# Kernel tuning notes

Measured on AMD Instinct MI355X. Metric: run time of the kernel, lower is better.

Reference implementation:

```python
import jax, jax.numpy as jnp
import numpy as np

B, S, H, D = 32, 512, 768, 64  # batch, seq_len, hidden_size, inner_dim
BIG = 1e12


def _rope(x, sin_pos, cos_pos):
    # x: [B,S,D]; rotate pairs: [-x1, x0, -x3, x2, ...]
    x2 = jnp.stack([-x[..., 1::2], x[..., ::2]], axis=-1).reshape(x.shape)
    return x * cos_pos + x2 * sin_pos


def setup_inputs() -> dict:
    key = jax.random.key(0)
    k1, k2, k3 = jax.random.split(key, 3)
    hidden = jax.random.normal(k1, (B, S, H), dtype=jnp.float32)
    attention_mask = jnp.ones((B, S), dtype=jnp.float32)
    span_ids = jax.random.randint(k2, (B, S, S), 0, 2).astype(jnp.int32)
    dense_w = jax.random.normal(k3, (H, 2 * D), dtype=jnp.float32) * 0.02
    dense_b = jnp.zeros((2 * D,), dtype=jnp.float32)
    return {"hidden": hidden, "attention_mask": attention_mask,
            "span_ids": span_ids, "dense_w": dense_w, "dense_b": dense_b}


def reference(hidden, attention_mask, span_ids, dense_w, dense_b):
    b, s, _ = hidden.shape
    out = hidden @ dense_w + dense_b            # [B,S,2D]
    qw, kw = out[..., :D], out[..., D:]
    # sinusoidal position embedding, interleaved [s0,c0,s1,c1,...]
    pos = jnp.arange(s, dtype=jnp.float32)[:, None]              # [S,1]
    inv_freq = 10000.0 ** (-2.0 * jnp.arange(D // 2, dtype=jnp.float32) / D)
    ang = pos * inv_freq                                         # [S,D/2]
    sin_pos = jnp.repeat(jnp.sin(ang), 2, axis=-1)[None]         # [1,S,D]
    cos_pos = jnp.repeat(jnp.cos(ang), 2, axis=-1)[None]
    qw = _rope(qw, sin_pos, cos_pos)
    kw = _rope(kw, sin_pos, cos_pos)
    logits = jnp.einsum('bmd,bnd->bmn', qw, kw)                  # [B,S,S]
    pad = attention_mask[:, None, :]                             # mask keys (n)
    logits = logits * pad - (1.0 - pad) * BIG
    tril = jnp.tril(jnp.ones((s, s), logits.dtype), -1)          # strict lower
    logits = logits - tril * BIG
    logits = logits / (D ** 0.5)
    # multilabel categorical crossentropy over rows [B*S, S]
    y_true = span_ids.astype(logits.dtype).reshape(b * s, -1)
    y_pred = logits.reshape(b * s, -1)
    yp = (1.0 - 2.0 * y_true) * y_pred
    zeros = jnp.zeros((b * s, 1), yp.dtype)
    y_neg = jnp.concatenate([yp - y_true * BIG, zeros], axis=-1)
    y_pos = jnp.concatenate([yp - (1.0 - y_true) * BIG, zeros], axis=-1)
    loss = (jax.nn.logsumexp(y_neg, axis=-1) + jax.nn.logsumexp(y_pos, axis=-1)).mean()
    return loss
```

## Files before the change

kernel.cpp:

```cpp
#include <hip/hip_runtime.h>
#include <hip/hip_bf16.h>
#include <math.h>

#define Bb   32
#define Ss   512
#define Hh   768
#define Dd   64
#define ND   128
#define Mrows (Bb*Ss)
#define BIGF 1.0e12f

typedef __attribute__((ext_vector_type(8))) short short8;
typedef __attribute__((ext_vector_type(4))) float floatx4;

__device__ __forceinline__ short f2bf(float x) {
    unsigned u = __builtin_bit_cast(unsigned, x);
    u = (u + 0x7FFF + ((u >> 16) & 1)) >> 16;
    return (short)u;
}

__global__ __launch_bounds__(256) void prep_kernel(
    const float* __restrict__ w, short* __restrict__ wT,
    float2* __restrict__ rt)
{
    int idx = blockIdx.x * 256 + threadIdx.x;
    int k = idx >> 7;
    int n = idx & 127;
    wT[n * Hh + k] = f2bf(w[idx]);
    if (idx < Ss * 32) {
        int spos = idx >> 5;
        int i    = idx & 31;
        float ln_base = -logf(10000.0f) / 32.0f;
        float invf = expf(ln_base * (float)i);
        float sn, cs;
        sincosf((float)spos * invf, &sn, &cs);
        rt[idx] = make_float2(sn, cs);
    }
}

__global__ __launch_bounds__(256) void proj_rope_kernel(
    const float*  __restrict__ hidden,
    const short*  __restrict__ wT,
    const float*  __restrict__ bias,
    const float2* __restrict__ rt,
    short* __restrict__ qbf,
    short* __restrict__ kbf)
{
    const int tid   = threadIdx.x;
    const int w     = tid >> 6;
    const int lane  = tid & 63;
    const int quad  = lane >> 4;
    const int l15   = lane & 15;
    const int h     = w & 1;
    const int mrow0 = blockIdx.x * 32 + (w >> 1) * 16;

    const float* ap  = hidden + (size_t)(mrow0 + l15) * Hh + quad * 8;
    const short* bp0 = wT + (size_t)(h * 64 + l15) * Hh + quad * 8;

    floatx4 acc[4] = {{0.f,0.f,0.f,0.f},{0.f,0.f,0.f,0.f},
                      {0.f,0.f,0.f,0.f},{0.f,0.f,0.f,0.f}};

    float4 A0[2], A1[2];
    short8 Bf[2][4];

#define PLOAD(buf, kofs) do {                                   \
    A0[buf] = *(const float4*)(ap + (kofs));                    \
    A1[buf] = *(const float4*)(ap + (kofs) + 4);                \
    Bf[buf][0] = *(const short8*)(bp0 + (kofs));                \
    Bf[buf][1] = *(const short8*)(bp0 + 16 * Hh + (kofs));      \
    Bf[buf][2] = *(const short8*)(bp0 + 32 * Hh + (kofs));      \
    Bf[buf][3] = *(const short8*)(bp0 + 48 * Hh + (kofs));      \
} while (0)

#define PCOMP(buf) do {                                         \
    short8 av;                                                  \
    av[0] = f2bf(A0[buf].x); av[1] = f2bf(A0[buf].y);           \
    av[2] = f2bf(A0[buf].z); av[3] = f2bf(A0[buf].w);           \
    av[4] = f2bf(A1[buf].x); av[5] = f2bf(A1[buf].y);           \
    av[6] = f2bf(A1[buf].z); av[7] = f2bf(A1[buf].w);           \
    acc[0] = __builtin_amdgcn_mfma_f32_16x16x32_bf16(av, Bf[buf][0], acc[0], 0, 0, 0); \
    acc[1] = __builtin_amdgcn_mfma_f32_16x16x32_bf16(av, Bf[buf][1], acc[1], 0, 0, 0); \
    acc[2] = __builtin_amdgcn_mfma_f32_16x16x32_bf16(av, Bf[buf][2], acc[2], 0, 0, 0); \
    acc[3] = __builtin_amdgcn_mfma_f32_16x16x32_bf16(av, Bf[buf][3], acc[3], 0, 0, 0); \
} while (0)

    PLOAD(0, 0);
    #pragma unroll
    for (int cc = 0; cc < 12; ++cc) {
        if (2 * cc + 1 < 24) PLOAD(1, (2 * cc + 1) * 32);
        PCOMP(0);
        if (2 * cc + 2 < 24) PLOAD(0, (2 * cc + 2) * 32);
        PCOMP(1);
    }
#undef PLOAD
#undef PCOMP

    short* dst = h ? kbf : qbf;
    const float* bptr = bias + h * 64;

    #pragma unroll
    for (int t = 0; t < 4; ++t) {
        const int d  = t * 16 + l15;
        const float bz = bptr[d];
        const float2* rtp = rt + (d >> 1);
        #pragma unroll
        for (int reg = 0; reg < 4; ++reg) {
            const int grow = mrow0 + quad * 4 + reg;
            const int spos = grow & (Ss - 1);
            float2 sc = rtp[spos * 32];
            float x  = acc[t][reg] + bz;
            float xo = __shfl_xor(x, 1);
            float o  = (d & 1) ? (x * sc.y + xo * sc.x)
                               : (x * sc.y - xo * sc.x);
            dst[(size_t)grow * Dd + d] = f2bf(o);
        }
    }
}

__global__ __launch_bounds__(512) void span_loss_kernel(
    const short* __restrict__ qbf,
    const short* __restrict__ kbf,
    const float* __restrict__ mask,
    const int*   __restrict__ span,
    double* __restrict__ rowsum)
{
    const int b    = blockIdx.x >> 4;
    const int m0   = (blockIdx.x & 15) * 32;
    const int tid  = threadIdx.x;
    const int w    = tid >> 6;
    const int lane = tid & 63;
    const int quad = lane >> 4;
    const int l15  = lane & 15;
    const int rh   = w & 1;
    const int cg   = w >> 1;
    const int rbase = m0 + rh * 16;
    const int cbase = cg * 128;

    __shared__ float part[2][4][32];
    __shared__ float bred[2][32];

    const short* qp = qbf + (size_t)(b * Ss + rbase + l15) * Dd + quad * 8;
    short8 a0 = *(const short8*)(qp);
    short8 a1 = *(const short8*)(qp + 32);

    floatx4 acc[8];
    #pragma unroll
    for (int t = 0; t < 8; ++t) acc[t] = (floatx4){0.f, 0.f, 0.f, 0.f};

    const short* kp = kbf + (size_t)(b * Ss + cbase + l15) * Dd + quad * 8;
    #pragma unroll
    for (int t = 0; t < 8; ++t) {
        short8 bv = *(const short8*)(kp + (size_t)t * 16 * Dd);
        acc[t] = __builtin_amdgcn_mfma_f32_16x16x32_bf16(a0, bv, acc[t], 0, 0, 0);
    }
    #pragma unroll
    for (int t = 0; t < 8; ++t) {
        short8 bv = *(const short8*)(kp + (size_t)t * 16 * Dd + 32);
        acc[t] = __builtin_amdgcn_mfma_f32_16x16x32_bf16(a1, bv, acc[t], 0, 0, 0);
    }

    unsigned spb = 0;
    #pragma unroll
    for (int t = 0; t < 8; ++t) {
        const int n = cbase + t * 16 + l15;
        const float pd = mask[b * Ss + n];
        #pragma unroll
        for (int reg = 0; reg < 4; ++reg) {
            const int m = rbase + quad * 4 + reg;
            const int sv = span[((size_t)(b * Ss + m)) * Ss + n];
            float logit = acc[t][reg] * pd - (1.0f - pd) * BIGF;
            if (n < m) logit -= BIGF;
            logit *= 0.125f;
            float ft = (float)sv;
            acc[t][reg] = (1.0f - 2.0f * ft) * logit;
            spb |= (unsigned)(sv != 0) << (t * 4 + reg);
        }
    }

    float mxn[4] = {0.f, 0.f, 0.f, 0.f};
    float mxp[4] = {0.f, 0.f, 0.f, 0.f};
    #pragma unroll
    for (int t = 0; t < 8; ++t) {
        #pragma unroll
        for (int reg = 0; reg < 4; ++reg) {
            float ft = (float)((spb >> (t * 4 + reg)) & 1u);
            float yp = acc[t][reg];
            mxn[reg] = fmaxf(mxn[reg], yp - ft * BIGF);
            mxp[reg] = fmaxf(mxp[reg], yp - (1.0f - ft) * BIGF);
        }
    }
    #pragma unroll
    for (int off = 1; off < 16; off <<= 1) {
        #pragma unroll
        for (int reg = 0; reg < 4; ++reg) {
            mxn[reg] = fmaxf(mxn[reg], __shfl_xor(mxn[reg], off));
            mxp[reg] = fmaxf(mxp[reg], __shfl_xor(mxp[reg], off));
        }
    }
    if (l15 == 0) {
        #pragma unroll
        for (int reg = 0; reg < 4; ++reg) {
            part[0][cg][rh * 16 + quad * 4 + reg] = mxn[reg];
            part[1][cg][rh * 16 + quad * 4 + reg] = mxp[reg];
        }
    }
    __syncthreads();
    if (tid < 64) {
        int np = tid >> 5, r = tid & 31;
        float mv = fmaxf(fmaxf(part[np][0][r], part[np][1][r]),
                         fmaxf(part[np][2][r], part[np][3][r]));
        bred[np][r] = mv;
    }
    __syncthreads();

    float bmn[4], bmp[4];
    #pragma unroll
    for (int reg = 0; reg < 4; ++reg) {
        bmn[reg] = bred[0][rh * 16 + quad * 4 + reg];
        bmp[reg] = bred[1][rh * 16 + quad * 4 + reg];
    }
    float smn[4] = {0.f, 0.f, 0.f, 0.f};
    float smp[4] = {0.f, 0.f, 0.f, 0.f};
    #pragma unroll
    for (int t = 0; t < 8; ++t) {
        #pragma unroll
        for (int reg = 0; reg < 4; ++reg) {
            float ft = (float)((spb >> (t * 4 + reg)) & 1u);
            float yp = acc[t][reg];
            smn[reg] += __expf(yp - ft * BIGF - bmn[reg]);
            smp[reg] += __expf(yp - (1.0f - ft) * BIGF - bmp[reg]);
        }
    }
    #pragma unroll
    for (int off = 1; off < 16; off <<= 1) {
        #pragma unroll
        for (int reg = 0; reg < 4; ++reg) {
            smn[reg] += __shfl_xor(smn[reg], off);
            smp[reg] += __shfl_xor(smp[reg], off);
        }
    }
    if (l15 == 0) {
        #pragma unroll
        for (int reg = 0; reg < 4; ++reg) {
            part[0][cg][rh * 16 + quad * 4 + reg] = smn[reg];
            part[1][cg][rh * 16 + quad * 4 + reg] = smp[reg];
        }
    }
    __syncthreads();

    if (tid < 32) {
        int r = tid;
        float SN = __expf(-bred[0][r])
                 + part[0][0][r] + part[0][1][r] + part[0][2][r] + part[0][3][r];
        float SP = __expf(-bred[1][r])
                 + part[1][0][r] + part[1][1][r] + part[1][2][r] + part[1][3][r];
        float lse = (bred[0][r] + logf(SN)) + (bred[1][r] + logf(SP));
        rowsum[(size_t)(b * Ss + m0 + r)] = (double)lse;
    }
}

__global__ __launch_bounds__(1024) void final_reduce_kernel(
    const double* __restrict__ rowsum, float* __restrict__ out)
{
    __shared__ double sh[1024];
    const int tid = threadIdx.x;
    double s = 0.0;
    #pragma unroll
    for (int i = 0; i < 16; ++i) s += rowsum[tid + i * 1024];
    sh[tid] = s;
    __syncthreads();
    for (int off = 512; off > 0; off >>= 1) {
        if (tid < off) sh[tid] += sh[tid + off];
        __syncthreads();
    }
    if (tid == 0) out[0] = (float)(sh[0] / (double)Mrows);
}

extern "C" void kernel_launch(void* const* d_in, const int* in_sizes, int n_in,
                              void* d_out, int out_size, void* d_ws, size_t ws_size,
                              hipStream_t stream)
{
    const float* hidden = (const float*)d_in[0];
    const float* mask   = (const float*)d_in[1];
    const int*   span   = (const int*)  d_in[2];
    const float* w      = (const float*)d_in[3];
    const float* bias   = (const float*)d_in[4];
    float* out = (float*)d_out;

    char* p = (char*)d_ws;
    double* rowsum = (double*)p;            p += 131072;
    short*  wT     = (short*)p;             p += 196608;
    float2* rt     = (float2*)p;            p += 131072;
    short*  qbf    = (short*)p;             p += (size_t)Mrows * Dd * 2;
    short*  kbf    = (short*)p;

    prep_kernel<<<Hh * ND / 256, 256, 0, stream>>>(w, wT, rt);
    proj_rope_kernel<<<Mrows / 32, 256, 0, stream>>>(hidden, wT, bias, rt, qbf, kbf);
    span_loss_kernel<<<Bb * 16, 512, 0, stream>>>(qbf, kbf, mask, span, rowsum);
    final_reduce_kernel<<<1, 1024, 0, stream>>>(rowsum, out);
}
```

Measured before the change: 158.5 us.

## Pre-swizzle weights into MFMA fragment order and prefetch span loads early

The prep kernel now writes the bf16 weights in the exact per-lane MFMA fragment layout, so each wave in the projection reads its B operand as one contiguous 1KB chunk per step instead of strided rows. The span loss kernel issues all span_ids and mask loads before the QK MFMAs, so the dominant span read overlaps with compute. Launch-bound occupancy hints are added to both kernels. Hoisting the span loads raises register pressure (32 ints per thread), which could conflict with the 4-block occupancy target.

```diff
diff --git a/kernel.cpp b/kernel.cpp
--- a/kernel.cpp
+++ b/kernel.cpp
@@ -20,13 +20,18 @@
 }
 
 __global__ __launch_bounds__(256) void prep_kernel(
-    const float* __restrict__ w, short* __restrict__ wT,
+    const float* __restrict__ w, short* __restrict__ wfrag,
     float2* __restrict__ rt)
 {
     int idx = blockIdx.x * 256 + threadIdx.x;
-    int k = idx >> 7;
-    int n = idx & 127;
-    wT[n * Hh + k] = f2bf(w[idx]);
+    int j    = idx & 7;
+    int lane = (idx >> 3) & 63;
+    int rest = idx >> 9;
+    int c    = rest % 24;
+    int tt   = rest / 24;
+    int n    = tt * 16 + (lane & 15);
+    int k    = c * 32 + (lane >> 4) * 8 + j;
+    wfrag[idx] = f2bf(w[k * ND + n]);
     if (idx < Ss * 32) {
         int spos = idx >> 5;
         int i    = idx & 31;
@@ -38,9 +43,9 @@
     }
 }
 
-__global__ __launch_bounds__(256) void proj_rope_kernel(
+__global__ __launch_bounds__(256, 2) void proj_rope_kernel(
     const float*  __restrict__ hidden,
-    const short*  __restrict__ wT,
+    const short*  __restrict__ wfrag,
     const float*  __restrict__ bias,
     const float2* __restrict__ rt,
     short* __restrict__ qbf,
@@ -55,7 +60,7 @@
     const int mrow0 = blockIdx.x * 32 + (w >> 1) * 16;
 
     const float* ap  = hidden + (size_t)(mrow0 + l15) * Hh + quad * 8;
-    const short* bp0 = wT + (size_t)(h * 64 + l15) * Hh + quad * 8;
+    const short* bp0 = wfrag + (size_t)(h * 4) * 24 * 512 + lane * 8;
 
     floatx4 acc[4] = {{0.f,0.f,0.f,0.f},{0.f,0.f,0.f,0.f},
                       {0.f,0.f,0.f,0.f},{0.f,0.f,0.f,0.f}};
@@ -63,13 +68,13 @@
     float4 A0[2], A1[2];
     short8 Bf[2][4];
 
-#define PLOAD(buf, kofs) do {                                   \
-    A0[buf] = *(const float4*)(ap + (kofs));                    \
-    A1[buf] = *(const float4*)(ap + (kofs) + 4);                \
-    Bf[buf][0] = *(const short8*)(bp0 + (kofs));                \
-    Bf[buf][1] = *(const short8*)(bp0 + 16 * Hh + (kofs));      \
-    Bf[buf][2] = *(const short8*)(bp0 + 32 * Hh + (kofs));      \
-    Bf[buf][3] = *(const short8*)(bp0 + 48 * Hh + (kofs));      \
+#define PLOAD(buf, c) do {                                        \
+    A0[buf] = *(const float4*)(ap + (c) * 32);                    \
+    A1[buf] = *(const float4*)(ap + (c) * 32 + 4);                \
+    Bf[buf][0] = *(const short8*)(bp0 + 0 * 24 * 512 + (c) * 512);\
+    Bf[buf][1] = *(const short8*)(bp0 + 1 * 24 * 512 + (c) * 512);\
+    Bf[buf][2] = *(const short8*)(bp0 + 2 * 24 * 512 + (c) * 512);\
+    Bf[buf][3] = *(const short8*)(bp0 + 3 * 24 * 512 + (c) * 512);\
 } while (0)
 
 #define PCOMP(buf) do {                                         \
@@ -87,9 +92,9 @@
     PLOAD(0, 0);
     #pragma unroll
     for (int cc = 0; cc < 12; ++cc) {
-        if (2 * cc + 1 < 24) PLOAD(1, (2 * cc + 1) * 32);
+        if (2 * cc + 1 < 24) PLOAD(1, 2 * cc + 1);
         PCOMP(0);
-        if (2 * cc + 2 < 24) PLOAD(0, (2 * cc + 2) * 32);
+        if (2 * cc + 2 < 24) PLOAD(0, 2 * cc + 2);
         PCOMP(1);
     }
 #undef PLOAD
@@ -117,7 +122,7 @@
     }
 }
 
-__global__ __launch_bounds__(512) void span_loss_kernel(
+__global__ __launch_bounds__(512, 4) void span_loss_kernel(
     const short* __restrict__ qbf,
     const short* __restrict__ kbf,
     const float* __restrict__ mask,
@@ -139,6 +144,20 @@
     __shared__ float part[2][4][32];
     __shared__ float bred[2][32];
 
+    int spv[8][4];
+    float pdv[8];
+    {
+        const int* spp = span + ((size_t)(b * Ss + rbase + quad * 4)) * Ss
+                              + cbase + l15;
+        #pragma unroll
+        for (int t = 0; t < 8; ++t) {
+            pdv[t] = mask[b * Ss + cbase + t * 16 + l15];
+            #pragma unroll
+            for (int reg = 0; reg < 4; ++reg)
+                spv[t][reg] = spp[(size_t)reg * Ss + t * 16];
+        }
+    }
+
     const short* qp = qbf + (size_t)(b * Ss + rbase + l15) * Dd + quad * 8;
     short8 a0 = *(const short8*)(qp);
     short8 a1 = *(const short8*)(qp + 32);
@@ -163,11 +182,11 @@
     #pragma unroll
     for (int t = 0; t < 8; ++t) {
         const int n = cbase + t * 16 + l15;
-        const float pd = mask[b * Ss + n];
+        const float pd = pdv[t];
         #pragma unroll
         for (int reg = 0; reg < 4; ++reg) {
             const int m = rbase + quad * 4 + reg;
-            const int sv = span[((size_t)(b * Ss + m)) * Ss + n];
+            const int sv = spv[t][reg];
             float logit = acc[t][reg] * pd - (1.0f - pd) * BIGF;
             if (n < m) logit -= BIGF;
             logit *= 0.125f;
@@ -289,13 +308,13 @@
 
     char* p = (char*)d_ws;
     double* rowsum = (double*)p;            p += 131072;
-    short*  wT     = (short*)p;             p += 196608;
+    short*  wfrag  = (short*)p;             p += 196608;
     float2* rt     = (float2*)p;            p += 131072;
     short*  qbf    = (short*)p;             p += (size_t)Mrows * Dd * 2;
     short*  kbf    = (short*)p;
 
-    prep_kernel<<<Hh * ND / 256, 256, 0, stream>>>(w, wT, rt);
-    proj_rope_kernel<<<Mrows / 32, 256, 0, stream>>>(hidden, wT, bias, rt, qbf, kbf);
+    prep_kernel<<<Hh * ND / 256, 256, 0, stream>>>(w, wfrag, rt);
+    proj_rope_kernel<<<Mrows / 32, 256, 0, stream>>>(hidden, wfrag, bias, rt, qbf, kbf);
     span_loss_kernel<<<Bb * 16, 512, 0, stream>>>(qbf, kbf, mask, span, rowsum);
     final_reduce_kernel<<<1, 1024, 0, stream>>>(rowsum, out);
 }
```

New measurement: 145.7 us. -8.0%, faster.
